# Performance work log

Measured on AMD Instinct MI355X. Metric: run time of the kernel, lower is better.

Reference implementation:

```python
import jax, jax.numpy as jnp
import numpy as np

TEMP = 0.05
MOMENTUM = 0.2
SMOOTH = 0.1
TAU_W = 0.09
NUM_SAMPLES = 100000
NUM_FEATURES = 256
BATCH = 256


def _l2norm(x, axis=1, eps=1e-12):
    return x / jnp.maximum(jnp.linalg.norm(x, axis=axis, keepdims=True), eps)


def setup_inputs() -> dict:
    key = jax.random.key(0)
    k1, k2, k3, k4 = jax.random.split(key, 4)
    inputs1 = jax.random.normal(k1, (BATCH, NUM_FEATURES), dtype=jnp.float32)
    inputs2 = jax.random.normal(k2, (BATCH, NUM_FEATURES), dtype=jnp.float32)
    features = jax.random.normal(k3, (NUM_SAMPLES, NUM_FEATURES), dtype=jnp.float32)
    features = _l2norm(features)  # memory bank holds unit-norm centroids
    targets = jax.random.randint(k4, (BATCH,), 0, NUM_SAMPLES)
    return {"inputs1": inputs1, "inputs2": inputs2, "features": features, "targets": targets}


def reference(inputs1, inputs2, features, targets):
    # ---- ClusterMemory.forward (mode='wgm') ----
    x1 = _l2norm(inputs1)                      # F.normalize(inputs1)
    x2 = _l2norm(inputs2)                      # F.normalize(inputs2)
    outputs = (x1 @ features.T) / TEMP         # [B, N] logits vs memory bank
    regression = (x2 @ features.T) / TEMP      # [B, N]

    logp = jax.nn.log_softmax(outputs, axis=1)
    # CrossEntropyLoss
    loss_c = -jnp.mean(jnp.take_along_axis(logp, targets[:, None], axis=1))
    # SoftEntropySmooth: smoothed mix of soft targets (detached) and one-hot
    onehot = jax.nn.one_hot(targets, features.shape[0], dtype=logp.dtype)
    smooth_t = jax.lax.stop_gradient(
        (1.0 - SMOOTH) * jax.nn.softmax(regression, axis=1) + SMOOTH * onehot
    )
    loss_s = jnp.sum(jnp.mean(-smooth_t * logp, axis=0))

    # ---- CM_WgtMean memory update: per-cluster segment softmax + scatter ----
    N = features.shape[0]
    d = jnp.sum(x1 * features[targets], axis=1)            # [B] sim to own centroid
    logits = -d / TAU_W
    segmax = jax.ops.segment_max(logits, targets, num_segments=N)   # [N]
    e = jnp.exp(logits - segmax[targets])                  # stable per-segment exp
    denom = jax.ops.segment_sum(e, targets, num_segments=N)
    w = e / denom[targets]                                 # segment softmax weights
    wmean = jax.ops.segment_sum(w[:, None] * x1, targets, num_segments=N)  # [N, D]
    counts = jax.ops.segment_sum(jnp.ones_like(d), targets, num_segments=N)
    upd = _l2norm(MOMENTUM * features + (1.0 - MOMENTUM) * wmean)
    new_features = jnp.where((counts > 0)[:, None], upd, features)

    return loss_c, loss_s, new_features
```

## Files before the change

kernel.cpp:

```cpp
#include <hip/hip_runtime.h>
#include <stdint.h>
#include <stddef.h>

#define TEMP      0.05f
#define INV_TEMP  20.0f
#define MOMENTUM  0.2f
#define SMOOTH    0.1f
#define TAU_W     0.09f
#define NSAMP     100000
#define NFEAT     256
#define BATCH     256
#define SHIFT     20.0f
#define MT        64
#define NSHADOW   16

typedef float  f32x4  __attribute__((ext_vector_type(4)));
typedef float  f32x2  __attribute__((ext_vector_type(2)));
typedef short  short8 __attribute__((ext_vector_type(8)));
typedef unsigned int u32x2 __attribute__((ext_vector_type(2)));

__device__ __forceinline__ short f2bf(float f) {
    uint32_t u = __builtin_bit_cast(uint32_t, f);
    u = (u + 0x7fffu + ((u >> 16) & 1u)) >> 16;
    return (short)u;
}

__device__ __forceinline__ void mfma_bf16(f32x4& c, short8 a, short8 b) {
    asm("v_mfma_f32_16x16x32_bf16 %0, %1, %2, %0" : "+v"(c) : "v"(a), "v"(b));
}

__device__ __forceinline__ float block_reduce_sum256(float v, float* scratch) {
    for (int o = 32; o > 0; o >>= 1) v += __shfl_down(v, o, 64);
    int lane = threadIdx.x & 63, wid = threadIdx.x >> 6;
    if (lane == 0) scratch[wid] = v;
    __syncthreads();
    if (threadIdx.x == 0)
        scratch[4] = scratch[0] + scratch[1] + scratch[2] + scratch[3];
    __syncthreads();
    return scratch[4];
}

__global__ void __launch_bounds__(256)
k_copy(const float* __restrict__ F, float* __restrict__ out) {
    const size_t total = (size_t)NSAMP * NFEAT / 4;
    size_t stride = (size_t)gridDim.x * 256;
    for (size_t i = (size_t)blockIdx.x * 256 + threadIdx.x; i < total; i += stride) {
        f32x4 v = *(const f32x4*)(F + i * 4);
        float* op = out + 2 + i * 4;
        __builtin_nontemporal_store(f32x2{v[0], v[1]}, (f32x2*)op);
        __builtin_nontemporal_store(f32x2{v[2], v[3]}, (f32x2*)(op + 2));
    }
}

__global__ void k_prep(const float* __restrict__ in1, const float* __restrict__ in2,
                       const float* __restrict__ F, const int* __restrict__ tgt,
                       float* __restrict__ x1n, short* __restrict__ Xb,
                       float* __restrict__ dvec, float* __restrict__ Zs) {
    __shared__ float scratch[8];
    int b = blockIdx.x;
    int k = threadIdx.x;
    int gid = b * NFEAT + k;
    if (gid < NSHADOW * BATCH * 3) Zs[gid] = 0.f;
    float v1 = in1[b * NFEAT + k];
    float v2 = in2[b * NFEAT + k];
    float n1 = block_reduce_sum256(v1 * v1, scratch);
    float n2 = block_reduce_sum256(v2 * v2, scratch);
    float x1 = v1 / fmaxf(sqrtf(n1), 1e-12f);
    float x2 = v2 / fmaxf(sqrtf(n2), 1e-12f);
    x1n[b * NFEAT + k] = x1;
    int g = b >> 5, r = b & 31;
    Xb[(g * 64 + r) * NFEAT + k]      = f2bf(x1);
    Xb[(g * 64 + 32 + r) * NFEAT + k] = f2bf(x2);
    int t = tgt[b];
    float dv = block_reduce_sum256(x1 * F[(size_t)t * NFEAT + k], scratch);
    if (k == 0) dvec[b] = dv;
}

__global__ void __launch_bounds__(512)
k_main(const float* __restrict__ F, const short* __restrict__ Xb,
       float* __restrict__ Zs) {
    __shared__ short lfs[MT * NFEAT];
    int tid = threadIdx.x;
    int m0 = blockIdx.x * MT;

    f32x4 v[8];
    #pragma unroll
    for (int rr = 0; rr < 8; ++rr) {
        int c   = rr * 512 + tid;
        int row = c >> 6, cc = c & 63;
        int grow = m0 + row;
        v[rr] = f32x4{0.f, 0.f, 0.f, 0.f};
        if (grow < NSAMP)
            v[rr] = *(const f32x4*)(F + (size_t)grow * NFEAT + cc * 4);
    }
    #pragma unroll
    for (int rr = 0; rr < 8; ++rr) {
        int c   = rr * 512 + tid;
        int row = c >> 6, cc = c & 63;
        uint32_t p0 = (uint32_t)(uint16_t)f2bf(v[rr][0]) | ((uint32_t)(uint16_t)f2bf(v[rr][1]) << 16);
        uint32_t p1 = (uint32_t)(uint16_t)f2bf(v[rr][2]) | ((uint32_t)(uint16_t)f2bf(v[rr][3]) << 16);
        int off = row * 512 + ((cc * 8) ^ ((row & 7) << 4));
        *(u32x2*)((char*)lfs + off) = (u32x2){p0, p1};
    }
    __syncthreads();

    int w = tid >> 6, lane = tid & 63;
    int l15 = lane & 15, lg = lane >> 4;

    f32x4 acc[4][4] = {};
    const short* xbase = Xb + (size_t)(w * 64) * NFEAT;

    #pragma unroll
    for (int kk = 0; kk < 8; ++kk) {
        int kb = kk * 64 + lg * 16;
        short8 a[4], bf[4];
        #pragma unroll
        for (int cf = 0; cf < 4; ++cf)
            bf[cf] = *(const short8*)(xbase + (cf * 16 + l15) * NFEAT + kk * 32 + lg * 8);
        #pragma unroll
        for (int mf = 0; mf < 4; ++mf) {
            int row = mf * 16 + l15;
            a[mf] = *(const short8*)((const char*)lfs + row * 512 + (kb ^ ((row & 7) << 4)));
        }
        #pragma unroll
        for (int mf = 0; mf < 4; ++mf)
            #pragma unroll
            for (int cf = 0; cf < 4; ++cf)
                mfma_bf16(acc[mf][cf], a[mf], bf[cf]);
    }

    int sh = (blockIdx.x & (NSHADOW - 1)) * BATCH;
    #pragma unroll
    for (int cf = 0; cf < 2; ++cf) {
        float z1 = 0.f, z2 = 0.f, s12 = 0.f;
        #pragma unroll
        for (int mf = 0; mf < 4; ++mf) {
            #pragma unroll
            for (int q = 0; q < 4; ++q) {
                int grow = m0 + mf * 16 + lg * 4 + q;
                if (grow < NSAMP) {
                    float l1 = acc[mf][cf][q] * INV_TEMP;
                    float e1 = __expf(l1 - SHIFT);
                    float e2 = __expf(acc[mf][cf + 2][q] * INV_TEMP - SHIFT);
                    z1 += e1; z2 += e2; s12 += e2 * l1;
                }
            }
        }
        z1  += __shfl_xor(z1, 16);  z1  += __shfl_xor(z1, 32);
        z2  += __shfl_xor(z2, 16);  z2  += __shfl_xor(z2, 32);
        s12 += __shfl_xor(s12, 16); s12 += __shfl_xor(s12, 32);
        if (lane < 16) {
            int b = w * 32 + cf * 16 + lane;
            atomicAdd(&Zs[sh + b], z1);
            atomicAdd(&Zs[NSHADOW * BATCH + sh + b], z2);
            atomicAdd(&Zs[2 * NSHADOW * BATCH + sh + b], s12);
        }
    }
}

__global__ void k_tail(const float* __restrict__ F, const int* __restrict__ tgt,
                       const float* __restrict__ dvec, const float* __restrict__ x1n,
                       const float* __restrict__ Zs, float* __restrict__ out) {
    __shared__ float scratch[8];
    if (blockIdx.x == BATCH) {
        int b = threadIdx.x;
        float z1 = 0.f, z2 = 0.f, s12 = 0.f;
        #pragma unroll
        for (int j = 0; j < NSHADOW; ++j) {
            z1  += Zs[j * BATCH + b];
            z2  += Zs[NSHADOW * BATCH + j * BATCH + b];
            s12 += Zs[2 * NSHADOW * BATCH + j * BATCH + b];
        }
        float L1   = SHIFT + logf(z1);
        float lpt  = dvec[b] * INV_TEMP - L1;
        float ce12 = s12 / z2;
        float lc = -lpt;
        float ls = (1.f - SMOOTH) * (L1 - ce12) + SMOOTH * (-lpt);
        float sc = block_reduce_sum256(lc, scratch);
        float ss = block_reduce_sum256(ls, scratch);
        if (b == 0) {
            out[0] = sc / (float)BATCH;
            out[1] = ss / (float)BATCH;
        }
        return;
    }
    __shared__ int   stgt[BATCH];
    __shared__ float slog[BATCH];
    int b = blockIdx.x, k = threadIdx.x;
    stgt[k] = tgt[k];
    slog[k] = -dvec[k] * (1.0f / TAU_W);
    __syncthreads();
    int t = stgt[b];
    for (int bp = 0; bp < b; ++bp)
        if (stgt[bp] == t) return;
    float m = -1e30f;
    for (int bp = 0; bp < BATCH; ++bp)
        if (stgt[bp] == t) m = fmaxf(m, slog[bp]);
    float denom = 0.f;
    for (int bp = 0; bp < BATCH; ++bp)
        if (stgt[bp] == t) denom += expf(slog[bp] - m);
    float wmean = 0.f;
    for (int bp = 0; bp < BATCH; ++bp)
        if (stgt[bp] == t)
            wmean += expf(slog[bp] - m) * x1n[bp * NFEAT + k];
    wmean /= denom;
    float upd = MOMENTUM * F[(size_t)t * NFEAT + k] + (1.f - MOMENTUM) * wmean;
    float nrm = block_reduce_sum256(upd * upd, scratch);
    out[2 + (size_t)t * NFEAT + k] = upd / fmaxf(sqrtf(nrm), 1e-12f);
}

extern "C" void kernel_launch(void* const* d_in, const int* in_sizes, int n_in,
                              void* d_out, int out_size, void* d_ws, size_t ws_size,
                              hipStream_t stream) {
    const float* in1 = (const float*)d_in[0];
    const float* in2 = (const float*)d_in[1];
    const float* F   = (const float*)d_in[2];
    const int*   tgt = (const int*)d_in[3];
    float* out = (float*)d_out;

    char* ws = (char*)d_ws;
    float* x1n = (float*)ws;
    short* Xb  = (short*)(ws + 262144);
    float* dv  = (float*)(ws + 524288);
    float* Zs  = (float*)(ws + 525312);

    hipLaunchKernelGGL(k_copy, dim3(2048), dim3(256), 0, stream, F, out);
    hipLaunchKernelGGL(k_prep, dim3(BATCH), dim3(256), 0, stream,
                       in1, in2, F, tgt, x1n, Xb, dv, Zs);
    hipLaunchKernelGGL(k_main, dim3((NSAMP + MT - 1) / MT), dim3(512), 0, stream,
                       F, Xb, Zs);
    hipLaunchKernelGGL(k_tail, dim3(BATCH + 1), dim3(256), 0, stream,
                       F, tgt, dv, x1n, Zs, out);
}
```

Before: 345.5 us.

## Pre-convert memory bank to fragment-ordered bf16 and stream tiles via global_load_lds

A new conversion kernel fuses the output copy of the feature bank with a bf16 conversion into an MFMA-fragment-ordered tiled buffer. The main GEMM kernel then loads each tile straight into LDS with global_load_lds and reads operands with conflict-free contiguous accesses, and the batch operand is likewise stored pre-swizzled. This removes the per-block fp32 load, conversion and swizzle work from the main kernel, at the cost of an extra write and read of a 51 MB bf16 copy. A fallback path uses the output buffer as scratch when the workspace is too small.

```diff
diff --git a/kernel.cpp b/kernel.cpp
--- a/kernel.cpp
+++ b/kernel.cpp
@@ -12,6 +12,7 @@
 #define BATCH     256
 #define SHIFT     20.0f
 #define MT        64
+#define TILES     1563
 #define NSHADOW   16
 
 typedef float  f32x4  __attribute__((ext_vector_type(4)));
@@ -29,6 +30,13 @@
     asm("v_mfma_f32_16x16x32_bf16 %0, %1, %2, %0" : "+v"(c) : "v"(a), "v"(b));
 }
 
+__device__ __forceinline__ void gload_lds16(const short* g, short* l) {
+    __builtin_amdgcn_global_load_lds(
+        (const __attribute__((address_space(1))) unsigned int*)(const void*)g,
+        (__attribute__((address_space(3))) unsigned int*)(void*)l,
+        16, 0, 0);
+}
+
 __device__ __forceinline__ float block_reduce_sum256(float v, float* scratch) {
     for (int o = 32; o > 0; o >>= 1) v += __shfl_down(v, o, 64);
     int lane = threadIdx.x & 63, wid = threadIdx.x >> 6;
@@ -38,6 +46,27 @@
         scratch[4] = scratch[0] + scratch[1] + scratch[2] + scratch[3];
     __syncthreads();
     return scratch[4];
+}
+
+__global__ void __launch_bounds__(256)
+k_conv(const float* __restrict__ F, short* __restrict__ Fb, float* outCopy) {
+    int t = threadIdx.x;
+    int row = blockIdx.x * 4 + (t >> 6);
+    int c4  = t & 63;
+    f32x4 v = {0.f, 0.f, 0.f, 0.f};
+    bool live = row < NSAMP;
+    if (live) v = *(const f32x4*)(F + (size_t)row * NFEAT + c4 * 4);
+    if (outCopy != nullptr && live) {
+        float* op = outCopy + 2 + (size_t)row * NFEAT + c4 * 4;
+        __builtin_nontemporal_store(f32x2{v[0], v[1]}, (f32x2*)op);
+        __builtin_nontemporal_store(f32x2{v[2], v[3]}, (f32x2*)(op + 2));
+    }
+    int tile = row >> 6, mf = (row >> 4) & 3, l15 = row & 15;
+    int kk = c4 >> 3, lg = (c4 >> 1) & 3, half = c4 & 1;
+    uint32_t p0 = (uint32_t)(uint16_t)f2bf(v[0]) | ((uint32_t)(uint16_t)f2bf(v[1]) << 16);
+    uint32_t p1 = (uint32_t)(uint16_t)f2bf(v[2]) | ((uint32_t)(uint16_t)f2bf(v[3]) << 16);
+    size_t off = (size_t)tile * 16384 + (size_t)(((kk * 4 + mf) * 64 + lg * 16 + l15) * 8) + half * 4;
+    *(u32x2*)(Fb + off) = (u32x2){p0, p1};
 }
 
 __global__ void __launch_bounds__(256)
@@ -54,7 +83,7 @@
 
 __global__ void k_prep(const float* __restrict__ in1, const float* __restrict__ in2,
                        const float* __restrict__ F, const int* __restrict__ tgt,
-                       float* __restrict__ x1n, short* __restrict__ Xb,
+                       float* __restrict__ x1n, short* __restrict__ XbF,
                        float* __restrict__ dvec, float* __restrict__ Zs) {
     __shared__ float scratch[8];
     int b = blockIdx.x;
@@ -68,65 +97,53 @@
     float x1 = v1 / fmaxf(sqrtf(n1), 1e-12f);
     float x2 = v2 / fmaxf(sqrtf(n2), 1e-12f);
     x1n[b * NFEAT + k] = x1;
-    int g = b >> 5, r = b & 31;
-    Xb[(g * 64 + r) * NFEAT + k]      = f2bf(x1);
-    Xb[(g * 64 + 32 + r) * NFEAT + k] = f2bf(x2);
+    int w = b >> 5, r = b & 31;
+    int cf = r >> 4, l15 = r & 15;
+    int kk = k >> 5, lg = (k >> 3) & 3, j = k & 7;
+    int lane = lg * 16 + l15;
+    XbF[(((w * 4 + cf) * 8 + kk) * 64 + lane) * 8 + j]     = f2bf(x1);
+    XbF[(((w * 4 + 2 + cf) * 8 + kk) * 64 + lane) * 8 + j] = f2bf(x2);
     int t = tgt[b];
     float dv = block_reduce_sum256(x1 * F[(size_t)t * NFEAT + k], scratch);
     if (k == 0) dvec[b] = dv;
 }
 
-__global__ void __launch_bounds__(512)
-k_main(const float* __restrict__ F, const short* __restrict__ Xb,
+__global__ void __launch_bounds__(512, 4)
+k_main(const short* __restrict__ Fb, const short* __restrict__ XbF,
        float* __restrict__ Zs) {
-    __shared__ short lfs[MT * NFEAT];
-    int tid = threadIdx.x;
+    __shared__ short lfs[16384];
+    int tid = threadIdx.x, w = tid >> 6, lane = tid & 63;
+    size_t tbase = (size_t)blockIdx.x * 16384;
+
+    #pragma unroll
+    for (int j = 0; j < 4; ++j)
+        gload_lds16(Fb + tbase + (size_t)((w * 4 + j) * 512 + lane * 8),
+                    &lfs[(w * 4 + j) * 512]);
+    __syncthreads();
+
+    int l15 = lane & 15, lg = lane >> 4;
     int m0 = blockIdx.x * MT;
-
-    f32x4 v[8];
-    #pragma unroll
-    for (int rr = 0; rr < 8; ++rr) {
-        int c   = rr * 512 + tid;
-        int row = c >> 6, cc = c & 63;
-        int grow = m0 + row;
-        v[rr] = f32x4{0.f, 0.f, 0.f, 0.f};
-        if (grow < NSAMP)
-            v[rr] = *(const f32x4*)(F + (size_t)grow * NFEAT + cc * 4);
-    }
-    #pragma unroll
-    for (int rr = 0; rr < 8; ++rr) {
-        int c   = rr * 512 + tid;
-        int row = c >> 6, cc = c & 63;
-        uint32_t p0 = (uint32_t)(uint16_t)f2bf(v[rr][0]) | ((uint32_t)(uint16_t)f2bf(v[rr][1]) << 16);
-        uint32_t p1 = (uint32_t)(uint16_t)f2bf(v[rr][2]) | ((uint32_t)(uint16_t)f2bf(v[rr][3]) << 16);
-        int off = row * 512 + ((cc * 8) ^ ((row & 7) << 4));
-        *(u32x2*)((char*)lfs + off) = (u32x2){p0, p1};
-    }
-    __syncthreads();
-
-    int w = tid >> 6, lane = tid & 63;
-    int l15 = lane & 15, lg = lane >> 4;
-
     f32x4 acc[4][4] = {};
-    const short* xbase = Xb + (size_t)(w * 64) * NFEAT;
+    const short* xw = XbF + (size_t)w * 16384 + lane * 8;
 
     #pragma unroll
     for (int kk = 0; kk < 8; ++kk) {
-        int kb = kk * 64 + lg * 16;
-        short8 a[4], bf[4];
-        #pragma unroll
-        for (int cf = 0; cf < 4; ++cf)
-            bf[cf] = *(const short8*)(xbase + (cf * 16 + l15) * NFEAT + kk * 32 + lg * 8);
-        #pragma unroll
-        for (int mf = 0; mf < 4; ++mf) {
-            int row = mf * 16 + l15;
-            a[mf] = *(const short8*)((const char*)lfs + row * 512 + (kb ^ ((row & 7) << 4)));
-        }
-        #pragma unroll
-        for (int mf = 0; mf < 4; ++mf)
-            #pragma unroll
-            for (int cf = 0; cf < 4; ++cf)
-                mfma_bf16(acc[mf][cf], a[mf], bf[cf]);
+        short8 bf0 = *(const short8*)(xw + (0 * 8 + kk) * 512);
+        short8 bf1 = *(const short8*)(xw + (1 * 8 + kk) * 512);
+        short8 bf2 = *(const short8*)(xw + (2 * 8 + kk) * 512);
+        short8 bf3 = *(const short8*)(xw + (3 * 8 + kk) * 512);
+        short8 a0 = *(const short8*)(&lfs[(kk * 4 + 0) * 512 + lane * 8]);
+        short8 a1 = *(const short8*)(&lfs[(kk * 4 + 1) * 512 + lane * 8]);
+        short8 a2 = *(const short8*)(&lfs[(kk * 4 + 2) * 512 + lane * 8]);
+        short8 a3 = *(const short8*)(&lfs[(kk * 4 + 3) * 512 + lane * 8]);
+        mfma_bf16(acc[0][0], a0, bf0); mfma_bf16(acc[0][1], a0, bf1);
+        mfma_bf16(acc[0][2], a0, bf2); mfma_bf16(acc[0][3], a0, bf3);
+        mfma_bf16(acc[1][0], a1, bf0); mfma_bf16(acc[1][1], a1, bf1);
+        mfma_bf16(acc[1][2], a1, bf2); mfma_bf16(acc[1][3], a1, bf3);
+        mfma_bf16(acc[2][0], a2, bf0); mfma_bf16(acc[2][1], a2, bf1);
+        mfma_bf16(acc[2][2], a2, bf2); mfma_bf16(acc[2][3], a2, bf3);
+        mfma_bf16(acc[3][0], a3, bf0); mfma_bf16(acc[3][1], a3, bf1);
+        mfma_bf16(acc[3][2], a3, bf2); mfma_bf16(acc[3][3], a3, bf3);
     }
 
     int sh = (blockIdx.x & (NSHADOW - 1)) * BATCH;
@@ -220,15 +237,28 @@
 
     char* ws = (char*)d_ws;
     float* x1n = (float*)ws;
-    short* Xb  = (short*)(ws + 262144);
+    short* XbF = (short*)(ws + 262144);
     float* dv  = (float*)(ws + 524288);
     float* Zs  = (float*)(ws + 525312);
-
-    hipLaunchKernelGGL(k_copy, dim3(2048), dim3(256), 0, stream, F, out);
-    hipLaunchKernelGGL(k_prep, dim3(BATCH), dim3(256), 0, stream,
-                       in1, in2, F, tgt, x1n, Xb, dv, Zs);
-    hipLaunchKernelGGL(k_main, dim3((NSAMP + MT - 1) / MT), dim3(512), 0, stream,
-                       F, Xb, Zs);
-    hipLaunchKernelGGL(k_tail, dim3(BATCH + 1), dim3(256), 0, stream,
-                       F, tgt, dv, x1n, Zs, out);
-}
+    const size_t FB_BYTES = (size_t)TILES * 32768;
+    const size_t NEED     = 589824 + FB_BYTES;
+
+    if (ws_size >= NEED) {
+        short* Fb = (short*)(ws + 589824);
+        hipLaunchKernelGGL(k_conv, dim3(TILES * 16), dim3(256), 0, stream, F, Fb, out);
+        hipLaunchKernelGGL(k_prep, dim3(BATCH), dim3(256), 0, stream,
+                           in1, in2, F, tgt, x1n, XbF, dv, Zs);
+        hipLaunchKernelGGL(k_main, dim3(TILES), dim3(512), 0, stream, Fb, XbF, Zs);
+        hipLaunchKernelGGL(k_tail, dim3(BATCH + 1), dim3(256), 0, stream,
+                           F, tgt, dv, x1n, Zs, out);
+    } else {
+        short* Fb = (short*)((char*)d_out + 51183616);
+        hipLaunchKernelGGL(k_conv, dim3(TILES * 16), dim3(256), 0, stream, F, Fb, (float*)nullptr);
+        hipLaunchKernelGGL(k_prep, dim3(BATCH), dim3(256), 0, stream,
+                           in1, in2, F, tgt, x1n, XbF, dv, Zs);
+        hipLaunchKernelGGL(k_main, dim3(TILES), dim3(512), 0, stream, Fb, XbF, Zs);
+        hipLaunchKernelGGL(k_copy, dim3(2048), dim3(256), 0, stream, F, out);
+        hipLaunchKernelGGL(k_tail, dim3(BATCH + 1), dim3(256), 0, stream,
+                           F, tgt, dv, x1n, Zs, out);
+    }
+}
```

Result: faster. 299.0 us (-13.5%).
